# Kernel optimization log

Measured on AMD Instinct MI355X. Metric: run time of the kernel, lower is better.

The kernel has to match this reference:

```python
import jax, jax.numpy as jnp
import numpy as np

N, E = 50000, 800000
F_IN, EDGE_DIM, H, C = 128, 64, 8, 32
NEG_SLOPE = 0.2


def setup_inputs() -> dict:
    key = jax.random.key(0)
    ks = jax.random.split(key, 9)
    return {
        "x": jax.random.normal(ks[0], (N, F_IN), dtype=jnp.float32),
        "edge_index": jax.random.randint(ks[1], (2, E), 0, N, dtype=jnp.int32),
        "edge_attr": jax.random.normal(ks[2], (E, EDGE_DIM), dtype=jnp.float32),
        "W": jax.random.normal(ks[3], (F_IN, H * C), dtype=jnp.float32) * 0.05,
        "att_src": jax.random.normal(ks[4], (H, C), dtype=jnp.float32) * 0.05,
        "att_dst": jax.random.normal(ks[5], (H, C), dtype=jnp.float32) * 0.05,
        "W_edge": jax.random.normal(ks[6], (EDGE_DIM, H * C), dtype=jnp.float32) * 0.05,
        "att_edge": jax.random.normal(ks[7], (H, C), dtype=jnp.float32) * 0.05,
        "bias": jax.random.normal(ks[8], (H * C,), dtype=jnp.float32) * 0.05,
    }


def reference(x, edge_index, edge_attr, W, att_src, att_dst, W_edge, att_edge, bias):
    src, dst = edge_index[0], edge_index[1]  # messages flow src -> dst
    # Pre-activation ReLU from Graph_intra.forward
    xr = jax.nn.relu(x)
    # Linear projection, per-head view: [N, H, C]
    xs = (xr @ W).reshape(N, H, C)
    # Per-node attention logits: [N, H]
    a_src = jnp.einsum("nhc,hc->nh", xs, att_src)
    a_dst = jnp.einsum("nhc,hc->nh", xs, att_dst)
    # Edge-feature attention contribution: [E, H]
    e_proj = (edge_attr @ W_edge).reshape(E, H, C)
    a_edge = jnp.einsum("ehc,hc->eh", e_proj, att_edge)
    # Per-edge logits + LeakyReLU
    alpha = jax.nn.leaky_relu(a_src[src] + a_dst[dst] + a_edge, NEG_SLOPE)  # [E, H]
    # Segment softmax over destination neighborhoods
    seg_max = jax.ops.segment_max(alpha, dst, num_segments=N)
    seg_max = jnp.where(jnp.isfinite(seg_max), seg_max, 0.0)
    alpha = jnp.exp(alpha - seg_max[dst])
    seg_sum = jax.ops.segment_sum(alpha, dst, num_segments=N)
    alpha = alpha / (seg_sum[dst] + 1e-16)
    # Weighted message aggregation: scatter-add alpha_e * x_src[e]
    msgs = alpha[:, :, None] * xs[src]  # [E, H, C]
    out = jax.ops.segment_sum(msgs, dst, num_segments=N)  # [N, H, C]
    return out.reshape(N, H * C) + bias
```

## Files before the change

kernel.cpp:

```cpp
#include <hip/hip_runtime.h>

#define N_NODES 50000
#define E_EDGES 800000
#define F_IN    128
#define EDGE_DIM 64
#define HC      256
#define NEG_SLOPE 0.2f

typedef __attribute__((ext_vector_type(8))) short short8;
typedef __attribute__((ext_vector_type(4))) float f32x4;

__device__ __forceinline__ unsigned short f2bf(float f) {
    unsigned u = __builtin_bit_cast(unsigned, f);
    u += 0x7fffu + ((u >> 16) & 1u);
    return (unsigned short)(u >> 16);
}
__device__ __forceinline__ float bf2f(unsigned short b) {
    return __builtin_bit_cast(float, (unsigned)b << 16);
}

__global__ __launch_bounds__(256) void k_pre(const float* __restrict__ W,
        const float* __restrict__ att_src, const float* __restrict__ att_dst,
        const float* __restrict__ W_edge, const float* __restrict__ att_edge,
        unsigned short* __restrict__ W_T, unsigned short* __restrict__ WaT,
        unsigned short* __restrict__ WaE, int* __restrict__ counts, int* __restrict__ gcur) {
    int idx = blockIdx.x * 256 + threadIdx.x;
    if (idx < N_NODES) counts[idx] = 0;
    if (idx == 0) *gcur = 0;
    if (idx < 32768) {
        int n = idx >> 7, k = idx & 127;
        W_T[n * 128 + k] = f2bf(W[k * 256 + n]);
    }
    if (idx < 2048) {
        int col = idx & 15, k = idx >> 4;
        const float* att = (col < 8) ? att_src : att_dst;
        int h = col & 7;
        float s = 0.f;
        #pragma unroll
        for (int c = 0; c < 32; ++c)
            s = fmaf(W[k * 256 + h * 32 + c], att[h * 32 + c], s);
        WaT[col * 128 + k] = f2bf(s);
    }
    if (idx < 1024) {
        int c = idx >> 6, k = idx & 63;
        float s = 0.f;
        if (c < 8) {
            #pragma unroll
            for (int cc = 0; cc < 32; ++cc)
                s = fmaf(W_edge[k * 256 + c * 32 + cc], att_edge[c * 32 + cc], s);
        }
        WaE[c * 64 + k] = (c < 8) ? f2bf(s) : (unsigned short)0;
    }
}

#define HIST_BLOCKS 782
#define ALOG_BLOCKS 782
__global__ __launch_bounds__(256) void kA(const float* __restrict__ x,
        const unsigned short* __restrict__ WaT,
        const int4* __restrict__ dst4, int* __restrict__ counts, int4* __restrict__ slot4,
        float* __restrict__ a_src, float* __restrict__ a_dst) {
    int t = threadIdx.x;
    if (blockIdx.x < HIST_BLOCKS) {
        int i = blockIdx.x * 256 + t;
        if (i < E_EDGES / 4) {
            int4 d = dst4[i];
            int4 sl;
            sl.x = atomicAdd(&counts[d.x], 1);
            sl.y = atomicAdd(&counts[d.y], 1);
            sl.z = atomicAdd(&counts[d.z], 1);
            sl.w = atomicAdd(&counts[d.w], 1);
            slot4[i] = sl;
        }
        return;
    }
    int tile = (blockIdx.x - HIST_BLOCKS) * 4 + (t >> 6);
    if (tile >= N_NODES / 16) return;
    int lane = t & 63, mr = lane & 15, g = lane >> 4;
    int node = tile * 16 + mr;
    f32x4 acc = (f32x4){0.f, 0.f, 0.f, 0.f};
    #pragma unroll
    for (int ks = 0; ks < 4; ++ks) {
        const float* xp = &x[(size_t)node * 128 + ks * 32 + g * 8];
        short8 a;
        #pragma unroll
        for (int j = 0; j < 8; ++j) a[j] = (short)f2bf(fmaxf(xp[j], 0.f));
        short8 b = *(const short8*)&WaT[mr * 128 + ks * 32 + g * 8];
        acc = __builtin_amdgcn_mfma_f32_16x16x32_bf16(a, b, acc, 0, 0, 0);
    }
    #pragma unroll
    for (int r = 0; r < 4; ++r) {
        int n2 = tile * 16 + g * 4 + r;
        if (mr < 8) a_src[n2 * 8 + mr]       = acc[r];
        else        a_dst[n2 * 8 + (mr - 8)] = acc[r];
    }
}

__global__ __launch_bounds__(256) void kB_alloc(const int* __restrict__ counts,
                                                int* __restrict__ starts,
                                                int* __restrict__ gcur) {
    int n = blockIdx.x * 256 + threadIdx.x;
    int c = (n < N_NODES) ? counts[n] : 0;
    int incl = c;
    #pragma unroll
    for (int off = 1; off < 64; off <<= 1) {
        int u = __shfl_up(incl, off);
        if ((threadIdx.x & 63) >= off) incl += u;
    }
    int total = __shfl(incl, 63);
    int wavebase = 0;
    if ((threadIdx.x & 63) == 63) wavebase = atomicAdd(gcur, total);
    wavebase = __shfl(wavebase, 63);
    if (n < N_NODES) starts[n] = wavebase + incl - c;
}

#define NT_TILES 782
#define GEMM_BLOCKS 512
__global__ __launch_bounds__(256) void kC(const float* __restrict__ x,
        const unsigned short* __restrict__ W_T, const unsigned short* __restrict__ WaE,
        const float* __restrict__ ea,
        const int* __restrict__ src, const int* __restrict__ dst,
        const int* __restrict__ slot, const int* __restrict__ starts,
        const float* __restrict__ a_src, const float* __restrict__ a_dst,
        unsigned short* __restrict__ xs,
        _Float16* __restrict__ w_perm, int* __restrict__ src_perm) {
    __shared__ __align__(16) char smem[32768];
    int t = threadIdx.x;

    if (blockIdx.x >= GEMM_BLOCKS) {
        int* s_sn  = (int*)smem;
        int* s_dn  = (int*)(smem + 1024);
        int* s_pos = (int*)(smem + 2048);
        int blockbase = (blockIdx.x - GEMM_BLOCKS) * 256;
        {
            int e = blockbase + t;
            int dn = dst[e], sn = src[e];
            int pos = starts[dn] + slot[e];
            s_sn[t] = sn; s_dn[t] = dn; s_pos[t] = pos;
            src_perm[pos] = sn;
        }
        __syncthreads();
        int lane = t & 63, w = t >> 6;
        int mr = lane & 15, g = lane >> 4;
        short8 b0 = *(const short8*)&WaE[mr * 64 + g * 8];
        short8 b1 = *(const short8*)&WaE[mr * 64 + 32 + g * 8];
        #pragma unroll
        for (int ti = 0; ti < 4; ++ti) {
            int lb = w * 64 + ti * 16;
            int er = blockbase + lb + mr;
            const float* ap = &ea[(size_t)er * 64 + g * 8];
            short8 a0, a1;
            #pragma unroll
            for (int j = 0; j < 8; ++j) a0[j] = (short)f2bf(ap[j]);
            #pragma unroll
            for (int j = 0; j < 8; ++j) a1[j] = (short)f2bf(ap[32 + j]);
            f32x4 acc = (f32x4){0.f, 0.f, 0.f, 0.f};
            acc = __builtin_amdgcn_mfma_f32_16x16x32_bf16(a0, b0, acc, 0, 0, 0);
            acc = __builtin_amdgcn_mfma_f32_16x16x32_bf16(a1, b1, acc, 0, 0, 0);
            if (mr < 8) {
                #pragma unroll
                for (int r = 0; r < 4; ++r) {
                    int le = lb + g * 4 + r;
                    int sn = s_sn[le], dn = s_dn[le];
                    float v = acc[r] + a_src[sn * 8 + mr] + a_dst[dn * 8 + mr];
                    v = (v > 0.f) ? v : NEG_SLOPE * v;
                    w_perm[(size_t)s_pos[le] * 8 + mr] = (_Float16)__expf(v);
                }
            }
        }
        return;
    }

    unsigned short* sB = (unsigned short*)smem;
    int ch = blockIdx.x >> 8;
    int rt0 = blockIdx.x & 255;
    for (int G = t; G < 2048; G += 256) {
        int nn = G >> 4, gi = G & 15;
        *(int4*)&sB[(nn * 16 + (gi ^ (nn & 7))) * 8] =
            *(const int4*)&W_T[(ch * 128 + nn) * 128 + gi * 8];
    }
    __syncthreads();
    int lane = t & 63, w = t >> 6, mr = lane & 15, g = lane >> 4;

    for (int rt = rt0; rt < NT_TILES; rt += 256) {
        int node = rt * 64 + w * 16 + mr;
        short8 a[4];
        if (node < N_NODES) {
            #pragma unroll
            for (int ks = 0; ks < 4; ++ks) {
                const float* xp = &x[(size_t)node * 128 + ks * 32 + g * 8];
                #pragma unroll
                for (int j = 0; j < 8; ++j) a[ks][j] = (short)f2bf(fmaxf(xp[j], 0.f));
            }
        } else {
            #pragma unroll
            for (int ks = 0; ks < 4; ++ks)
                #pragma unroll
                for (int j = 0; j < 8; ++j) a[ks][j] = 0;
        }

        f32x4 acc[8];
        #pragma unroll
        for (int i = 0; i < 8; ++i) acc[i] = (f32x4){0.f, 0.f, 0.f, 0.f};

        #pragma unroll
        for (int ks = 0; ks < 4; ++ks) {
            int pos = (ks * 4 + g) ^ (mr & 7);
            #pragma unroll
            for (int nt = 0; nt < 8; ++nt) {
                short8 b = *(const short8*)&sB[((nt * 16 + mr) * 16 + pos) * 8];
                acc[nt] = __builtin_amdgcn_mfma_f32_16x16x32_bf16(a[ks], b, acc[nt], 0, 0, 0);
            }
        }

        #pragma unroll
        for (int r = 0; r < 4; ++r) {
            int node2 = rt * 64 + w * 16 + g * 4 + r;
            if (node2 < N_NODES) {
                #pragma unroll
                for (int nt = 0; nt < 8; ++nt)
                    xs[(size_t)node2 * 256 + ch * 128 + nt * 16 + mr] = f2bf(acc[nt][r]);
            }
        }
    }
}

__global__ __launch_bounds__(256) void k6_wave(
    const int* __restrict__ starts, const int* __restrict__ counts,
    const _Float16* __restrict__ w_perm, const int* __restrict__ src_perm,
    const unsigned short* __restrict__ xs, const float* __restrict__ bias,
    float* __restrict__ out) {
    int lane = threadIdx.x & 63;
    int n = blockIdx.x * 4 + (threadIdx.x >> 6);
    if (n >= N_NODES) return;
    int start = starts[n], cnt = counts[n];
    int j = lane >> 3;
    int hq = lane >> 3;

    float acc0 = 0.f, acc1 = 0.f, acc2 = 0.f, acc3 = 0.f;
    float psum = 0.f;
    for (int base = 0; base < cnt; base += 8) {
        int nk = cnt - base; if (nk > 8) nk = 8;
        float wv = (float)w_perm[(size_t)(start + base) * 8 + lane];
        if (j >= nk) wv = 0.f;
        psum += wv;
        int sv = src_perm[start + base + (lane & 7)];
        #pragma unroll
        for (int jj = 0; jj < 8; ++jj) {
            int s = __shfl(sv, jj);
            s = (jj < nk) ? s : 0;
            float w = __shfl(wv, jj * 8 + hq);
            ushort4 xv = *(const ushort4*)&xs[(size_t)s * 256 + lane * 4];
            acc0 = fmaf(w, bf2f(xv.x), acc0);
            acc1 = fmaf(w, bf2f(xv.y), acc1);
            acc2 = fmaf(w, bf2f(xv.z), acc2);
            acc3 = fmaf(w, bf2f(xv.w), acc3);
        }
    }
    psum += __shfl_xor(psum, 8);
    psum += __shfl_xor(psum, 16);
    psum += __shfl_xor(psum, 32);
    float denom = __shfl(psum, hq);
    float rinv = 1.0f / (denom + 1e-16f);
    float4 bv = *(const float4*)&bias[lane * 4];
    f32x4 o;
    o[0] = acc0 * rinv + bv.x;
    o[1] = acc1 * rinv + bv.y;
    o[2] = acc2 * rinv + bv.z;
    o[3] = acc3 * rinv + bv.w;
    __builtin_nontemporal_store(o, (f32x4*)&out[(size_t)n * 256 + lane * 4]);
}

extern "C" void kernel_launch(void* const* d_in, const int* in_sizes, int n_in,
                              void* d_out, int out_size, void* d_ws, size_t ws_size,
                              hipStream_t stream) {
    const float* x         = (const float*)d_in[0];
    const int*   ei        = (const int*)d_in[1];
    const float* edge_attr = (const float*)d_in[2];
    const float* W         = (const float*)d_in[3];
    const float* att_src   = (const float*)d_in[4];
    const float* att_dst   = (const float*)d_in[5];
    const float* W_edge    = (const float*)d_in[6];
    const float* att_edge  = (const float*)d_in[7];
    const float* bias      = (const float*)d_in[8];
    float* out = (float*)d_out;

    const int* e_src = ei;
    const int* e_dst = ei + E_EDGES;

    char* p = (char*)d_ws;
    unsigned short* xs = (unsigned short*)p; p += (size_t)N_NODES * HC * 2;
    float* a_src   = (float*)p; p += (size_t)N_NODES * 8 * 4;
    float* a_dst   = (float*)p; p += (size_t)N_NODES * 8 * 4;
    _Float16* w_perm = (_Float16*)p; p += (size_t)E_EDGES * 8 * 2 + 256;
    int* src_perm  = (int*)p;   p += (size_t)E_EDGES * 4 + 256;
    int* slot      = (int*)p;   p += (size_t)E_EDGES * 4 + 256;
    unsigned short* W_T  = (unsigned short*)p; p += 32768 * 2;
    unsigned short* WaT  = (unsigned short*)p; p += 2048 * 2;
    unsigned short* WaE  = (unsigned short*)p; p += 1024 * 2;
    int* counts    = (int*)p;   p += 200192;
    int* starts    = (int*)p;   p += 200192;
    int* gcur      = (int*)p;   p += 256;

    hipLaunchKernelGGL(k_pre, dim3(196), dim3(256), 0, stream,
                       W, att_src, att_dst, W_edge, att_edge, W_T, WaT, WaE, counts, gcur);
    hipLaunchKernelGGL(kA, dim3(HIST_BLOCKS + ALOG_BLOCKS), dim3(256), 0, stream,
                       x, WaT, (const int4*)e_dst, counts, (int4*)slot, a_src, a_dst);
    hipLaunchKernelGGL(kB_alloc, dim3(196), dim3(256), 0, stream,
                       counts, starts, gcur);
    hipLaunchKernelGGL(kC, dim3(GEMM_BLOCKS + E_EDGES / 256), dim3(256), 0, stream,
                       x, W_T, WaE, edge_attr, e_src, e_dst, slot, starts,
                       a_src, a_dst, xs, w_perm, src_perm);
    hipLaunchKernelGGL(k6_wave, dim3(N_NODES / 4), dim3(256), 0, stream,
                       starts, counts, w_perm, src_perm, xs, bias, out);
}
```

Before: 209.9 us.

## Split edge permutation into own kernel, stage weights in LDS, widen gather loads

Moves the computation of each edge's permuted position and the src_perm scatter into a separate kernel kB2. The edge-logit blocks now read that precomputed position and stage the eight fp16 head weights in shared memory. Each edge's weights then go out as one 16-byte store instead of eight scattered 2-byte stores. The aggregation kernel now processes two edges per iteration with each half-wave loading 16 bytes of xs, then combines the halves with a cross-half shuffle. The cost is an extra launch, an extra pos array round-trip through memory, and half the lanes idle during the output store.

```diff
diff --git a/kernel.cpp b/kernel.cpp
--- a/kernel.cpp
+++ b/kernel.cpp
@@ -113,16 +113,29 @@
     if (n < N_NODES) starts[n] = wavebase + incl - c;
 }
 
+__global__ __launch_bounds__(256) void kB2(const int* __restrict__ dst,
+        const int* __restrict__ slot, const int* __restrict__ starts,
+        const int* __restrict__ src, int* __restrict__ pos, int* __restrict__ src_perm) {
+    int e = blockIdx.x * 1024 + threadIdx.x;
+    #pragma unroll
+    for (int i = 0; i < 4; ++i, e += 256) {
+        if (e < E_EDGES) {
+            int p = starts[dst[e]] + slot[e];
+            pos[e] = p;
+            src_perm[p] = src[e];
+        }
+    }
+}
+
 #define NT_TILES 782
 #define GEMM_BLOCKS 512
 __global__ __launch_bounds__(256) void kC(const float* __restrict__ x,
         const unsigned short* __restrict__ W_T, const unsigned short* __restrict__ WaE,
         const float* __restrict__ ea,
-        const int* __restrict__ src, const int* __restrict__ dst,
-        const int* __restrict__ slot, const int* __restrict__ starts,
+        const int* __restrict__ src, const int* __restrict__ pos,
         const float* __restrict__ a_src, const float* __restrict__ a_dst,
-        unsigned short* __restrict__ xs,
-        _Float16* __restrict__ w_perm, int* __restrict__ src_perm) {
+        const int* __restrict__ dst,
+        unsigned short* __restrict__ xs, _Float16* __restrict__ w_perm) {
     __shared__ __align__(16) char smem[32768];
     int t = threadIdx.x;
 
@@ -130,13 +143,13 @@
         int* s_sn  = (int*)smem;
         int* s_dn  = (int*)(smem + 1024);
         int* s_pos = (int*)(smem + 2048);
+        _Float16* s_w = (_Float16*)(smem + 3072);
         int blockbase = (blockIdx.x - GEMM_BLOCKS) * 256;
         {
             int e = blockbase + t;
-            int dn = dst[e], sn = src[e];
-            int pos = starts[dn] + slot[e];
-            s_sn[t] = sn; s_dn[t] = dn; s_pos[t] = pos;
-            src_perm[pos] = sn;
+            s_sn[t] = src[e];
+            s_dn[t] = dst[e];
+            s_pos[t] = pos[e];
         }
         __syncthreads();
         int lane = t & 63, w = t >> 6;
@@ -163,10 +176,12 @@
                     int sn = s_sn[le], dn = s_dn[le];
                     float v = acc[r] + a_src[sn * 8 + mr] + a_dst[dn * 8 + mr];
                     v = (v > 0.f) ? v : NEG_SLOPE * v;
-                    w_perm[(size_t)s_pos[le] * 8 + mr] = (_Float16)__expf(v);
+                    s_w[le * 8 + mr] = (_Float16)__expf(v);
                 }
             }
         }
+        __syncthreads();
+        *(int4*)&w_perm[(size_t)s_pos[t] * 8] = *(const int4*)&s_w[t * 8];
         return;
     }
 
@@ -204,10 +219,10 @@
 
         #pragma unroll
         for (int ks = 0; ks < 4; ++ks) {
-            int pos = (ks * 4 + g) ^ (mr & 7);
+            int posk = (ks * 4 + g) ^ (mr & 7);
             #pragma unroll
             for (int nt = 0; nt < 8; ++nt) {
-                short8 b = *(const short8*)&sB[((nt * 16 + mr) * 16 + pos) * 8];
+                short8 b = *(const short8*)&sB[((nt * 16 + mr) * 16 + posk) * 8];
                 acc[nt] = __builtin_amdgcn_mfma_f32_16x16x32_bf16(a[ks], b, acc[nt], 0, 0, 0);
             }
         }
@@ -234,10 +249,15 @@
     if (n >= N_NODES) return;
     int start = starts[n], cnt = counts[n];
     int j = lane >> 3;
-    int hq = lane >> 3;
-
-    float acc0 = 0.f, acc1 = 0.f, acc2 = 0.f, acc3 = 0.f;
+    int l5 = lane & 31;
+    int h2 = lane >> 5;
+    int hq = l5 >> 2;
+
+    float acc[8];
+    #pragma unroll
+    for (int k = 0; k < 8; ++k) acc[k] = 0.f;
     float psum = 0.f;
+
     for (int base = 0; base < cnt; base += 8) {
         int nk = cnt - base; if (nk > 8) nk = 8;
         float wv = (float)w_perm[(size_t)(start + base) * 8 + lane];
@@ -245,29 +265,41 @@
         psum += wv;
         int sv = src_perm[start + base + (lane & 7)];
         #pragma unroll
-        for (int jj = 0; jj < 8; ++jj) {
-            int s = __shfl(sv, jj);
-            s = (jj < nk) ? s : 0;
-            float w = __shfl(wv, jj * 8 + hq);
-            ushort4 xv = *(const ushort4*)&xs[(size_t)s * 256 + lane * 4];
-            acc0 = fmaf(w, bf2f(xv.x), acc0);
-            acc1 = fmaf(w, bf2f(xv.y), acc1);
-            acc2 = fmaf(w, bf2f(xv.z), acc2);
-            acc3 = fmaf(w, bf2f(xv.w), acc3);
-        }
-    }
+        for (int jj = 0; jj < 8; jj += 2) {
+            int eidx = jj + h2;
+            int s = __shfl(sv, eidx);
+            s = (eidx < nk) ? s : 0;
+            float w = __shfl(wv, eidx * 8 + hq);
+            int4 xv = *(const int4*)&xs[(size_t)s * 256 + l5 * 8];
+            acc[0] = fmaf(w, bf2f((unsigned short)(xv.x & 0xffff)), acc[0]);
+            acc[1] = fmaf(w, bf2f((unsigned short)((unsigned)xv.x >> 16)), acc[1]);
+            acc[2] = fmaf(w, bf2f((unsigned short)(xv.y & 0xffff)), acc[2]);
+            acc[3] = fmaf(w, bf2f((unsigned short)((unsigned)xv.y >> 16)), acc[3]);
+            acc[4] = fmaf(w, bf2f((unsigned short)(xv.z & 0xffff)), acc[4]);
+            acc[5] = fmaf(w, bf2f((unsigned short)((unsigned)xv.z >> 16)), acc[5]);
+            acc[6] = fmaf(w, bf2f((unsigned short)(xv.w & 0xffff)), acc[6]);
+            acc[7] = fmaf(w, bf2f((unsigned short)((unsigned)xv.w >> 16)), acc[7]);
+        }
+    }
+    #pragma unroll
+    for (int k = 0; k < 8; ++k) acc[k] += __shfl_xor(acc[k], 32);
     psum += __shfl_xor(psum, 8);
     psum += __shfl_xor(psum, 16);
     psum += __shfl_xor(psum, 32);
     float denom = __shfl(psum, hq);
     float rinv = 1.0f / (denom + 1e-16f);
-    float4 bv = *(const float4*)&bias[lane * 4];
-    f32x4 o;
-    o[0] = acc0 * rinv + bv.x;
-    o[1] = acc1 * rinv + bv.y;
-    o[2] = acc2 * rinv + bv.z;
-    o[3] = acc3 * rinv + bv.w;
-    __builtin_nontemporal_store(o, (f32x4*)&out[(size_t)n * 256 + lane * 4]);
+
+    if (h2 == 0) {
+        const float* bp = &bias[l5 * 8];
+        f32x4 o0, o1;
+        #pragma unroll
+        for (int k = 0; k < 4; ++k) o0[k] = acc[k] * rinv + bp[k];
+        #pragma unroll
+        for (int k = 0; k < 4; ++k) o1[k] = acc[4 + k] * rinv + bp[4 + k];
+        float* op = &out[(size_t)n * 256 + l5 * 8];
+        __builtin_nontemporal_store(o0, (f32x4*)op);
+        __builtin_nontemporal_store(o1, (f32x4*)(op + 4));
+    }
 }
 
 extern "C" void kernel_launch(void* const* d_in, const int* in_sizes, int n_in,
@@ -294,6 +326,7 @@
     _Float16* w_perm = (_Float16*)p; p += (size_t)E_EDGES * 8 * 2 + 256;
     int* src_perm  = (int*)p;   p += (size_t)E_EDGES * 4 + 256;
     int* slot      = (int*)p;   p += (size_t)E_EDGES * 4 + 256;
+    int* pos       = (int*)p;   p += (size_t)E_EDGES * 4 + 256;
     unsigned short* W_T  = (unsigned short*)p; p += 32768 * 2;
     unsigned short* WaT  = (unsigned short*)p; p += 2048 * 2;
     unsigned short* WaE  = (unsigned short*)p; p += 1024 * 2;
@@ -307,9 +340,11 @@
                        x, WaT, (const int4*)e_dst, counts, (int4*)slot, a_src, a_dst);
     hipLaunchKernelGGL(kB_alloc, dim3(196), dim3(256), 0, stream,
                        counts, starts, gcur);
+    hipLaunchKernelGGL(kB2, dim3((E_EDGES + 1023) / 1024), dim3(256), 0, stream,
+                       e_dst, slot, starts, e_src, pos, src_perm);
     hipLaunchKernelGGL(kC, dim3(GEMM_BLOCKS + E_EDGES / 256), dim3(256), 0, stream,
-                       x, W_T, WaE, edge_attr, e_src, e_dst, slot, starts,
-                       a_src, a_dst, xs, w_perm, src_perm);
+                       x, W_T, WaE, edge_attr, e_src, pos, a_src, a_dst, e_dst,
+                       xs, w_perm);
     hipLaunchKernelGGL(k6_wave, dim3(N_NODES / 4), dim3(256), 0, stream,
                        starts, counts, w_perm, src_perm, xs, bias, out);
 }
```

After: 211.4 us. About the same (+0.7%).
